# Kernel optimization log

Hardware: AMD Instinct MI355X
Metric: run time of the kernel (lower is better)

The kernel has to match this reference:

```python
import jax, jax.numpy as jnp
import numpy as np

MULTI_INFER_NUM = 8
D_EMBED = 128
N_LAYERS = 2
T, B = 2048, 32


def setup_inputs() -> dict:
    key = jax.random.key(0)
    k1, k2, k3, k4 = jax.random.split(key, 4)
    positions = jax.random.randint(k1, (T, B), 0, 16, dtype=jnp.int64)
    outputs = jax.random.normal(k2, (T, B, D_EMBED), dtype=jnp.float32)
    # 4 LinearTransferFeatures per layer (self_forget, logit, logit_forget, out_forget)
    Ws = jax.random.normal(k3, (N_LAYERS, 4, MULTI_INFER_NUM + 1, D_EMBED, D_EMBED), dtype=jnp.float32) * 0.05
    bs = jax.random.normal(k4, (N_LAYERS, 4, MULTI_INFER_NUM + 1, D_EMBED), dtype=jnp.float32) * 0.05
    return {"positions": positions, "outputs": outputs, "Ws": Ws, "bs": bs}


def _linear(x, onehot, W, b):
    # x: [t,b,d]; onehot: [t,b,e]; W: [e,d,f]; b: [e,d]
    # Equivalent to gathering W[r_pos] ([t,b,d,f]) then einsum('ibde,ibd->ibe'),
    # but computed as per-expert GEMMs + one-hot combine (grouped-GEMM form).
    y_all = jnp.einsum('tbd,edf->tbef', x, W)      # per-expert outputs
    y = jnp.einsum('tbef,tbe->tbf', y_all, onehot)  # select token's expert
    return y + jnp.einsum('tbe,ed->tbd', onehot, b)


def reference(positions, outputs, Ws, bs):
    m = Ws.shape[2] - 1  # multi_infer_num
    r_pos = jnp.where(positions < m, positions, m)
    onehot = jax.nn.one_hot(r_pos, m + 1, dtype=outputs.dtype)
    x = outputs
    for l in range(Ws.shape[0]):
        self_forget = _linear(x, onehot, Ws[l, 0], bs[l, 0])
        logit = _linear(x, onehot, Ws[l, 1], bs[l, 1])
        logit_forget = _linear(x, onehot, Ws[l, 2], bs[l, 2])
        out_forget = _linear(x, onehot, Ws[l, 3], bs[l, 3])
        new_res = x * jax.nn.sigmoid(self_forget) + jnp.tanh(logit) * jax.nn.sigmoid(logit_forget)
        x = jnp.tanh(new_res) * jax.nn.sigmoid(out_forget)
    return x
```

## Files before the change

kernel.cpp:

```cpp
#include <hip/hip_runtime.h>
#include <hip/hip_fp16.h>
#include <stdint.h>

#define TOKENS 65536
#define D      128
#define NEXP   9
#define MT     64
#define MAXTILES (TOKENS / MT + NEXP)
#define NHB    256

typedef _Float16 f16;
typedef _Float16 f16x8  __attribute__((ext_vector_type(8)));
typedef float    f32x4  __attribute__((ext_vector_type(4)));
typedef uint32_t u32;

#define WI_TOKOFF  32
#define WI_TILEOFF 48
#define WI_HIST    128
#define WI_BBASE   2432
#define WI_PERM    4736
#define WS_WF_OFF  ((4736 + TOKENS) * 4)

#define LOG2E  1.44269504f
__device__ __forceinline__ float sigm(float v) {
  return __builtin_amdgcn_rcpf(1.0f + __builtin_amdgcn_exp2f(-LOG2E * v));
}
__device__ __forceinline__ float tanh_fast(float v) {
  return 1.0f - 2.0f * __builtin_amdgcn_rcpf(__builtin_amdgcn_exp2f(2.0f * LOG2E * v) + 1.0f);
}

__global__ void k_prep(const float* __restrict__ Ws, const int* __restrict__ pos,
                       int* __restrict__ wsI, f16* __restrict__ Wf) {
  const int tid = threadIdx.x;
  if (blockIdx.x < 288) {
    const int mat = blockIdx.x >> 2;
    const int q   = blockIdx.x & 3;
    const float* src = Ws + (size_t)mat * (D * D);
    f16* dst = Wf + (size_t)mat * (D * D);
#pragma unroll
    for (int p = 0; p < 2; ++p) {
      int cc = q * 512 + p * 256 + tid;
      int ln = cc & 63;
      int kb = (cc >> 6) & 3;
      int c  = cc >> 8;
      int quad = ln >> 4, n = ln & 15;
      int f  = c * 16 + n;
      int d0 = kb * 32 + quad * 8;
      f16x8 w;
#pragma unroll
      for (int i = 0; i < 8; ++i) w[i] = (f16)src[(d0 + i) * D + f];
      *(f16x8*)(dst + cc * 8) = w;
    }
  } else {
    const int b = blockIdx.x - 288;
    __shared__ int h[NEXP];
    if (tid < NEXP) h[tid] = 0;
    __syncthreads();
    int e = pos[b * 256 + tid]; e = e < 8 ? e : 8;
    atomicAdd(&h[e], 1);
    __syncthreads();
    if (tid < NEXP) wsI[WI_HIST + b * NEXP + tid] = h[tid];
  }
}

__global__ void k_scan(int* __restrict__ wsI) {
  const int tid = threadIdx.x;
  const int lane = tid & 63, w = tid >> 6;
  __shared__ int wsum[4];
  __shared__ int totalsS[NEXP];
  __shared__ int tokoffS[NEXP + 1];
  int rel[NEXP];
  int myh[NEXP];
#pragma unroll
  for (int e = 0; e < NEXP; ++e) myh[e] = wsI[WI_HIST + tid * NEXP + e];

  for (int e = 0; e < NEXP; ++e) {
    int v = myh[e];
    int x = v;
#pragma unroll
    for (int off = 1; off < 64; off <<= 1) {
      int y = __shfl_up(x, off);
      if (lane >= off) x += y;
    }
    if (lane == 63) wsum[w] = x;
    __syncthreads();
    int add = 0;
    for (int w2 = 0; w2 < w; ++w2) add += wsum[w2];
    int incl = x + add;
    rel[e] = incl - v;
    if (tid == 255) totalsS[e] = incl;
    __syncthreads();
  }
  if (tid == 0) {
    int tok = 0, tile = 0;
    wsI[WI_TOKOFF] = 0; wsI[WI_TILEOFF] = 0; tokoffS[0] = 0;
    for (int e = 0; e < NEXP; ++e) {
      int cnt = totalsS[e];
      tok += cnt; tile += (cnt + MT - 1) / MT;
      wsI[WI_TOKOFF + e + 1] = tok;  tokoffS[e + 1] = tok;
      wsI[WI_TILEOFF + e + 1] = tile;
    }
  }
  __syncthreads();
#pragma unroll
  for (int e = 0; e < NEXP; ++e)
    wsI[WI_BBASE + tid * NEXP + e] = tokoffS[e] + rel[e];
}

__global__ void k_assign(const int* __restrict__ pos, int* __restrict__ wsI) {
  const int tid = threadIdx.x, b = blockIdx.x;
  const int lane = tid & 63, w = tid >> 6;
  int e = pos[b * 256 + tid]; e = e < 8 ? e : 8;
  __shared__ int waveCnt[4][NEXP];
  __shared__ int waveBase[4][NEXP];
  int myRank = 0;
#pragma unroll
  for (int ee = 0; ee < NEXP; ++ee) {
    unsigned long long m = __ballot(e == ee);
    if (e == ee) myRank = __popcll(m & ((1ull << lane) - 1ull));
    if (lane == 0) waveCnt[w][ee] = __popcll(m);
  }
  __syncthreads();
  if (tid < NEXP) {
    int s = 0;
#pragma unroll
    for (int w2 = 0; w2 < 4; ++w2) { waveBase[w2][tid] = s; s += waveCnt[w2][tid]; }
  }
  __syncthreads();
  int base = wsI[WI_BBASE + b * NEXP + e];
  wsI[WI_PERM + base + waveBase[w][e] + myRank] = b * 256 + tid;
}

__launch_bounds__(256, 4)
__global__ void k_main(const float* __restrict__ xin, const float* __restrict__ bsPtr,
                       const int* __restrict__ wsI, const f16* __restrict__ Wf,
                       float* __restrict__ outPtr) {
  __shared__ __attribute__((aligned(16))) f16 Ash[MT][136];
  __shared__ int s_tok[MT];

  const int tid = threadIdx.x;
  const int bid = blockIdx.x;
  const int ntiles = wsI[WI_TILEOFF + NEXP];
  if (bid >= ntiles) return;

  int e = 0, tileOffE = 0;
#pragma unroll
  for (int ee = 0; ee < NEXP; ee++) {
    int to = wsI[WI_TILEOFF + ee];
    if (to <= bid) { e = ee; tileOffE = to; }
  }
  const int tokStart = wsI[WI_TOKOFF + e] + (bid - tileOffE) * MT;
  const int tokEnd   = wsI[WI_TOKOFF + e + 1];
  const int rowsValid = min(MT, tokEnd - tokStart);

  {
    int m = tid >> 2, h = tid & 3;
    bool valid = (m < rowsValid);
    int tok = 0;
    if (valid) tok = wsI[WI_PERM + tokStart + m];
    if (h == 0) s_tok[m] = valid ? tok : -1;
    const float4* src = (const float4*)(xin + (size_t)tok * D + h * 32);
    f16* drow = &Ash[m][h * 32];
#pragma unroll
    for (int i = 0; i < 4; i++) {
      float4 a = make_float4(0.f, 0.f, 0.f, 0.f), b2 = a;
      if (valid) { a = src[2 * i]; b2 = src[2 * i + 1]; }
      f16x8 wv;
      wv[0] = (f16)a.x;  wv[1] = (f16)a.y;  wv[2] = (f16)a.z;  wv[3] = (f16)a.w;
      wv[4] = (f16)b2.x; wv[5] = (f16)b2.y; wv[6] = (f16)b2.z; wv[7] = (f16)b2.w;
      *(f16x8*)&drow[i * 8] = wv;
    }
  }
  __syncthreads();

  const int lane = tid & 63;
  const int n    = lane & 15;
  const int quad = lane >> 4;
  const int rowBase = (tid >> 6) * 16;
  const int vlane = lane * 8;
  const f16* We = Wf + (size_t)e * 16384;

  f16x8 aF[4];
  f16x8 b0[4], b1[4];
  f32x4 acc0, acc1, acc2, acc3;

#define PREFETCH_B(BUF, LL, CC, JJ)                                            \
  do {                                                                         \
    if ((LL) < 2) {                                                            \
      const f16* _p = We + ((LL) * 4 + (JJ)) * 147456 + (CC) * 2048 + vlane;   \
      _Pragma("unroll")                                                        \
      for (int _kb = 0; _kb < 4; ++_kb)                                        \
        BUF[_kb] = *(const f16x8*)(_p + _kb * 512);                            \
    }                                                                          \
  } while (0)

#define MFMA_GROUP(ACC, BUF)                                                   \
  do {                                                                         \
    f32x4 _a = {0.f, 0.f, 0.f, 0.f};                                           \
    _Pragma("unroll") for (int _kb = 0; _kb < 4; ++_kb)                        \
      _a = __builtin_amdgcn_mfma_f32_16x16x32_f16(aF[_kb], BUF[_kb], _a, 0, 0, 0); \
    ACC = _a;                                                                  \
  } while (0)

  PREFETCH_B(b0, 0, 0, 0);

#pragma unroll 1
  for (int l = 0; l < 2; l++) {
    {
      int mA = rowBase + n;
#pragma unroll
      for (int kb = 0; kb < 4; kb++)
        aF[kb] = *(const f16x8*)&Ash[mA][kb * 32 + quad * 8];
    }
#pragma unroll 1
    for (int c = 0; c < 8; c++) {
      const int f = c * 16 + n;
      float bias[4];
#pragma unroll
      for (int j = 0; j < 4; j++)
        bias[j] = bsPtr[((l * 4 + j) * NEXP + e) * D + f];

      const int ln = (c == 7) ? l + 1 : l;
      const int cn = (c + 1) & 7;

      PREFETCH_B(b1, l, c, 1);   MFMA_GROUP(acc0, b0);
      PREFETCH_B(b0, l, c, 2);   MFMA_GROUP(acc1, b1);
      PREFETCH_B(b1, l, c, 3);   MFMA_GROUP(acc2, b0);
      PREFETCH_B(b0, ln, cn, 0); MFMA_GROUP(acc3, b1);

#pragma unroll
      for (int r = 0; r < 4; r++) {
        int m = rowBase + quad * 4 + r;
        float sf = acc0[r] + bias[0];
        float lg = acc1[r] + bias[1];
        float lf = acc2[r] + bias[2];
        float of = acc3[r] + bias[3];
        float xv = (float)Ash[m][f];
        float nr = xv * sigm(sf) + tanh_fast(lg) * sigm(lf);
        float xn = tanh_fast(nr) * sigm(of);
        if (l == 0) {
          Ash[m][f] = (f16)xn;
        } else {
          int tok = s_tok[m];
          if (tok >= 0) outPtr[(size_t)tok * D + f] = xn;
        }
      }
    }
  }
#undef PREFETCH_B
#undef MFMA_GROUP
}

extern "C" void kernel_launch(void* const* d_in, const int* in_sizes, int n_in,
                              void* d_out, int out_size, void* d_ws, size_t ws_size,
                              hipStream_t stream) {
  const int*   pos = (const int*)d_in[0];
  const float* x   = (const float*)d_in[1];
  const float* Ws  = (const float*)d_in[2];
  const float* bs  = (const float*)d_in[3];
  float* out = (float*)d_out;
  int* wsI = (int*)d_ws;
  f16* Wf = (f16*)((char*)d_ws + WS_WF_OFF);

  k_prep  <<<544, 256, 0, stream>>>(Ws, pos, wsI, Wf);
  k_scan  <<<1, 256, 0, stream>>>(wsI);
  k_assign<<<NHB, 256, 0, stream>>>(pos, wsI);
  k_main  <<<MAXTILES, 256, 0, stream>>>(x, bs, wsI, Wf, out);
}
```

Measured before the change: 145.9 us.

## Halve token tile and split output columns across waves instead of rows

Shrinks the per-block token tile from 64 to 32 rows and changes the work split so each wave owns two 16-column output chunks across all 32 rows, rather than 16 rows across all columns. Each wave now loads only a quarter of the expert weight columns per layer, cutting the weight traffic per block, and the number of blocks doubles, which raises parallelism. The price is a block-wide barrier between layers (needed because layer-0 results written by other waves feed the next layer's A fragments) and more tiles overall, so weights are re-read more times across the grid.

```diff
diff --git a/kernel.cpp b/kernel.cpp
--- a/kernel.cpp
+++ b/kernel.cpp
@@ -5,7 +5,7 @@
 #define TOKENS 65536
 #define D      128
 #define NEXP   9
-#define MT     64
+#define MT     32
 #define MAXTILES (TOKENS / MT + NEXP)
 #define NHB    256
 
@@ -154,15 +154,15 @@
   const int rowsValid = min(MT, tokEnd - tokStart);
 
   {
-    int m = tid >> 2, h = tid & 3;
+    int m = tid >> 3, h = tid & 7;
     bool valid = (m < rowsValid);
     int tok = 0;
     if (valid) tok = wsI[WI_PERM + tokStart + m];
     if (h == 0) s_tok[m] = valid ? tok : -1;
-    const float4* src = (const float4*)(xin + (size_t)tok * D + h * 32);
-    f16* drow = &Ash[m][h * 32];
-#pragma unroll
-    for (int i = 0; i < 4; i++) {
+    const float4* src = (const float4*)(xin + (size_t)tok * D + h * 16);
+    f16* drow = &Ash[m][h * 16];
+#pragma unroll
+    for (int i = 0; i < 2; i++) {
       float4 a = make_float4(0.f, 0.f, 0.f, 0.f), b2 = a;
       if (valid) { a = src[2 * i]; b2 = src[2 * i + 1]; }
       f16x8 wv;
@@ -176,13 +176,22 @@
   const int lane = tid & 63;
   const int n    = lane & 15;
   const int quad = lane >> 4;
-  const int rowBase = (tid >> 6) * 16;
+  const int cBase = (tid >> 6) * 2;
   const int vlane = lane * 8;
   const f16* We = Wf + (size_t)e * 16384;
 
-  f16x8 aF[4];
+  f16x8 aF0[4], aF1[4];
   f16x8 b0[4], b1[4];
-  f32x4 acc0, acc1, acc2, acc3;
+  f32x4 acc[4][2];
+
+#define LOAD_AF()                                                              \
+  do {                                                                         \
+    _Pragma("unroll")                                                          \
+    for (int _kb = 0; _kb < 4; ++_kb) {                                        \
+      aF0[_kb] = *(const f16x8*)&Ash[n][_kb * 32 + quad * 8];                  \
+      aF1[_kb] = *(const f16x8*)&Ash[16 + n][_kb * 32 + quad * 8];             \
+    }                                                                          \
+  } while (0)
 
 #define PREFETCH_B(BUF, LL, CC, JJ)                                            \
   do {                                                                         \
@@ -194,61 +203,69 @@
     }                                                                          \
   } while (0)
 
-#define MFMA_GROUP(ACC, BUF)                                                   \
+#define MFMA2(G, BUF)                                                          \
   do {                                                                         \
-    f32x4 _a = {0.f, 0.f, 0.f, 0.f};                                           \
-    _Pragma("unroll") for (int _kb = 0; _kb < 4; ++_kb)                        \
-      _a = __builtin_amdgcn_mfma_f32_16x16x32_f16(aF[_kb], BUF[_kb], _a, 0, 0, 0); \
-    ACC = _a;                                                                  \
+    f32x4 _x = {0.f, 0.f, 0.f, 0.f}, _y = {0.f, 0.f, 0.f, 0.f};                \
+    _Pragma("unroll")                                                          \
+    for (int _kb = 0; _kb < 4; ++_kb) {                                        \
+      _x = __builtin_amdgcn_mfma_f32_16x16x32_f16(aF0[_kb], BUF[_kb], _x, 0, 0, 0); \
+      _y = __builtin_amdgcn_mfma_f32_16x16x32_f16(aF1[_kb], BUF[_kb], _y, 0, 0, 0); \
+    }                                                                          \
+    acc[G][0] = _x; acc[G][1] = _y;                                            \
   } while (0)
 
-  PREFETCH_B(b0, 0, 0, 0);
+  PREFETCH_B(b0, 0, cBase, 0);
+  LOAD_AF();
+  __syncthreads();
 
 #pragma unroll 1
   for (int l = 0; l < 2; l++) {
-    {
-      int mA = rowBase + n;
-#pragma unroll
-      for (int kb = 0; kb < 4; kb++)
-        aF[kb] = *(const f16x8*)&Ash[mA][kb * 32 + quad * 8];
-    }
 #pragma unroll 1
-    for (int c = 0; c < 8; c++) {
-      const int f = c * 16 + n;
+    for (int ci = 0; ci < 2; ci++) {
+      const int cc = cBase + ci;
+      const int f = cc * 16 + n;
       float bias[4];
 #pragma unroll
       for (int j = 0; j < 4; j++)
         bias[j] = bsPtr[((l * 4 + j) * NEXP + e) * D + f];
 
-      const int ln = (c == 7) ? l + 1 : l;
-      const int cn = (c + 1) & 7;
-
-      PREFETCH_B(b1, l, c, 1);   MFMA_GROUP(acc0, b0);
-      PREFETCH_B(b0, l, c, 2);   MFMA_GROUP(acc1, b1);
-      PREFETCH_B(b1, l, c, 3);   MFMA_GROUP(acc2, b0);
-      PREFETCH_B(b0, ln, cn, 0); MFMA_GROUP(acc3, b1);
-
-#pragma unroll
-      for (int r = 0; r < 4; r++) {
-        int m = rowBase + quad * 4 + r;
-        float sf = acc0[r] + bias[0];
-        float lg = acc1[r] + bias[1];
-        float lf = acc2[r] + bias[2];
-        float of = acc3[r] + bias[3];
-        float xv = (float)Ash[m][f];
-        float nr = xv * sigm(sf) + tanh_fast(lg) * sigm(lf);
-        float xn = tanh_fast(nr) * sigm(of);
-        if (l == 0) {
-          Ash[m][f] = (f16)xn;
-        } else {
-          int tok = s_tok[m];
-          if (tok >= 0) outPtr[(size_t)tok * D + f] = xn;
+      const int ln = (ci == 1) ? l + 1 : l;
+      const int cn = (ci == 1) ? cBase : cc + 1;
+
+      PREFETCH_B(b1, l, cc, 1);  MFMA2(0, b0);
+      PREFETCH_B(b0, l, cc, 2);  MFMA2(1, b1);
+      PREFETCH_B(b1, l, cc, 3);  MFMA2(2, b0);
+      PREFETCH_B(b0, ln, cn, 0); MFMA2(3, b1);
+
+#pragma unroll
+      for (int s = 0; s < 2; s++) {
+#pragma unroll
+        for (int r = 0; r < 4; r++) {
+          int m = s * 16 + quad * 4 + r;
+          float sf = acc[0][s][r] + bias[0];
+          float lg = acc[1][s][r] + bias[1];
+          float lf = acc[2][s][r] + bias[2];
+          float of = acc[3][s][r] + bias[3];
+          float xv = (float)Ash[m][f];
+          float nr = xv * sigm(sf) + tanh_fast(lg) * sigm(lf);
+          float xn = tanh_fast(nr) * sigm(of);
+          if (l == 0) {
+            Ash[m][f] = (f16)xn;
+          } else {
+            int tok = s_tok[m];
+            if (tok >= 0) outPtr[(size_t)tok * D + f] = xn;
+          }
         }
       }
     }
-  }
+    if (l == 0) {
+      __syncthreads();
+      LOAD_AF();
+    }
+  }
+#undef LOAD_AF
 #undef PREFETCH_B
-#undef MFMA_GROUP
+#undef MFMA2
 }
 
 extern "C" void kernel_launch(void* const* d_in, const int* in_sizes, int n_in,
```

Measured after the change: 133.7 us. -8.4%, faster.
